# Optimization experiments

Measured on AMD Instinct MI355X. Metric: run time of the kernel, lower is better.

The kernel has to match this reference:

```python
import jax, jax.numpy as jnp
import numpy as np

N, J, P = 512, 20000, 8   # samples, genes (rna_count), covariates
DIM = J - 1               # pivot=True drops one column from the softmax logits


def setup_inputs() -> dict:
    key = jax.random.key(0)
    k0, k1, k2, k3, k4 = jax.random.split(key, 5)
    X = jax.random.normal(k0, (N, P), dtype=jnp.float32)
    # counts: non-negative integers stored as float (matches torch float64 Y of counts)
    Y = jnp.round(jax.random.uniform(k1, (N, J), dtype=jnp.float32) * 1000.0)
    mu = jax.random.normal(k2, (DIM,), dtype=jnp.float32)
    beta = jax.random.normal(k3, (P * DIM,), dtype=jnp.float32) * 0.1
    phi = jax.random.normal(k4, (J,), dtype=jnp.float32)
    return {"mu": mu, "beta": beta, "phi": phi, "X": X, "Y": Y}


def _nb_loglik(y, mean, disp):
    # NB with mean `mean` and dispersion `disp` (var = mean + disp*mean^2):
    # r = 1/disp, p = r/(r+mean)
    # log pmf = lgamma(y+r) - lgamma(r) - lgamma(y+1) + r*log(p) + y*log(1-p)
    r = 1.0 / disp
    log_rpm = jnp.log(r + mean)
    return (jax.lax.lgamma(y + r) - jax.lax.lgamma(r) - jax.lax.lgamma(y + 1.0)
            + r * (jnp.log(r) - log_rpm)
            + y * (jnp.log(mean) - log_rpm))


def reference(mu, beta, phi, X, Y):
    n, p = X.shape
    dim = mu.shape[0]
    beta_ = beta.reshape(p, dim)
    logits = mu + X @ beta_                                   # [N, J-1]
    logits = jnp.concatenate(
        [logits, jnp.zeros((n, 1), dtype=logits.dtype)], axis=1)  # pivot column of zeros -> [N, J]
    pi = jax.nn.softmax(logits, axis=1)                       # exp(logits - logsumexp)
    s = jnp.sum(Y, axis=1, keepdims=True)                     # [N, 1] total counts per sample
    mean = s * pi                                             # [N, J]
    disp = jax.nn.softplus(phi)                               # [J]
    log_lik = jnp.sum(_nb_loglik(Y, mean, disp))
    return log_lik.reshape(1)
```

## Files before the change

### kernel.cpp

```cpp
#include <hip/hip_runtime.h>

constexpr int N_SAMPLES = 512;
constexpr int J_GENES   = 20000;
constexpr int P_COV     = 8;
constexpr int DIM       = J_GENES - 1;
constexpr int BLOCK     = 256;
constexpr int NW        = BLOCK / 64;
constexpr int CHUNK     = 2048;
constexpr int NBJ       = 10;
constexpr int JPAD      = NBJ * CHUNK;
constexpr int NPART     = NBJ * N_SAMPLES;
constexpr int TABLE_N   = 1024;

constexpr size_t WS_RW    = 0;
constexpr size_t WS_MUP   = WS_RW    + JPAD;
constexpr size_t WS_BETAP = WS_MUP   + JPAD;
constexpr size_t WS_CVEC  = WS_BETAP + (size_t)P_COV * JPAD;
constexpr size_t WS_LGYT  = WS_CVEC  + JPAD;
constexpr size_t WS_SACC  = WS_LGYT  + TABLE_N;
constexpr size_t WS_EACC  = WS_SACC  + N_SAMPLES;
constexpr size_t WS_PART  = WS_EACC  + N_SAMPLES;
constexpr size_t WS_TOTAL = WS_PART  + NPART;

__device__ inline float wave_reduce_sum(float v) {
#pragma unroll
    for (int off = 32; off > 0; off >>= 1)
        v += __shfl_down(v, off, 64);
    return v;
}

__device__ inline float block_reduce_sum(float v, float* red) {
    const int t = threadIdx.x;
    float w = wave_reduce_sum(v);
    if ((t & 63) == 0) red[t >> 6] = w;
    __syncthreads();
    float b = 0.0f;
#pragma unroll
    for (int i = 0; i < NW; ++i) b += red[i];
    return b;
}

__device__ inline float lgamma_pos(float z) {
    float corr = 0.0f;
    if (z < 8.0f) {
        float p = z;
        p *= (z + 1.0f); p *= (z + 2.0f); p *= (z + 3.0f);
        p *= (z + 4.0f); p *= (z + 5.0f); p *= (z + 6.0f); p *= (z + 7.0f);
        corr = -__logf(p);
        z += 8.0f;
    }
    float lz  = __logf(z);
    float rz  = __builtin_amdgcn_rcpf(z);
    float rz2 = rz * rz;
    float ser = rz * fmaf(rz2, fmaf(rz2, 7.9365079365e-4f, -2.7777777778e-3f),
                          8.3333333333e-2f);
    return fmaf(z - 0.5f, lz, 0.91893853320467274f - z + ser + corr);
}

__device__ inline float4 logits4(const float* __restrict__ ws,
                                 const float* __restrict__ x, int j) {
    float4 lg = *(const float4*)(ws + WS_MUP + j);
#pragma unroll
    for (int p = 0; p < P_COV; ++p) {
        float4 bb = *(const float4*)(ws + WS_BETAP + (size_t)p * JPAD + j);
        lg.x = fmaf(x[p], bb.x, lg.x);
        lg.y = fmaf(x[p], bb.y, lg.y);
        lg.z = fmaf(x[p], bb.z, lg.z);
        lg.w = fmaf(x[p], bb.w, lg.w);
    }
    return lg;
}

__global__ __launch_bounds__(BLOCK) void prep_kernel(
    const float* __restrict__ mu, const float* __restrict__ beta,
    const float* __restrict__ phi, float* __restrict__ ws) {
    const int gid = blockIdx.x * BLOCK + threadIdx.x;
    if (gid < TABLE_N) ws[WS_LGYT + gid] = lgammaf((float)gid + 1.0f);
    if (gid < N_SAMPLES) { ws[WS_SACC + gid] = 0.0f; ws[WS_EACC + gid] = 0.0f; }
    if (gid >= JPAD) return;
    if (gid < J_GENES) {
        const int j = gid;
        float ph = phi[j];
        float sp = (ph > 20.0f) ? ph : log1pf(__expf(ph));
        float r  = 1.0f / sp;
        ws[WS_RW   + j] = r;
        ws[WS_CVEC + j] = fmaf(r, -__logf(sp), -lgammaf(r));
        ws[WS_MUP  + j] = (j < DIM) ? mu[j] : 0.0f;
#pragma unroll
        for (int p = 0; p < P_COV; ++p)
            ws[WS_BETAP + (size_t)p * JPAD + j] =
                (j < DIM) ? beta[p * DIM + j] : 0.0f;
    } else {
        ws[WS_RW   + gid] = 1.0f;
        ws[WS_CVEC + gid] = 0.0f;
        ws[WS_MUP  + gid] = 0.0f;
#pragma unroll
        for (int p = 0; p < P_COV; ++p)
            ws[WS_BETAP + (size_t)p * JPAD + gid] = 0.0f;
    }
}

__global__ __launch_bounds__(BLOCK) void rowsum_kernel(
    const float* __restrict__ X, const float* __restrict__ Y,
    float* __restrict__ ws) {
    const int n = blockIdx.y;
    const int t = threadIdx.x;
    const int j0 = blockIdx.x * CHUNK + t * 4;

    float x[P_COV];
#pragma unroll
    for (int p = 0; p < P_COV; ++p) x[p] = X[n * P_COV + p];
    const float* yrow = Y + (size_t)n * J_GENES;

    float s_acc = 0.0f, e_acc = 0.0f;
    for (int g = 0; g < 2; ++g) {
        const int j = j0 + g * (BLOCK * 4);
        if (j < J_GENES) {
            float4 y4 = *(const float4*)(yrow + j);
            float4 lg = logits4(ws, x, j);
            s_acc += (y4.x + y4.y) + (y4.z + y4.w);
            e_acc += (__expf(lg.x) + __expf(lg.y)) + (__expf(lg.z) + __expf(lg.w));
        }
    }

    __shared__ float red[NW];
    float s = block_reduce_sum(s_acc, red);
    __syncthreads();
    float e = block_reduce_sum(e_acc, red);
    if (t == 0) {
        atomicAdd(&ws[WS_SACC + n], s);
        atomicAdd(&ws[WS_EACC + n], e);
    }
}

__global__ __launch_bounds__(BLOCK) void loglik_kernel(
    const float* __restrict__ X, const float* __restrict__ Y,
    float* __restrict__ ws) {
    const int n = blockIdx.y;
    const int t = threadIdx.x;
    const int j0 = blockIdx.x * CHUNK + t * 4;

    __shared__ __align__(16) float tbl[TABLE_N];
    *(float4*)&tbl[t * 4] = *(const float4*)(ws + WS_LGYT + t * 4);

    float x[P_COV];
#pragma unroll
    for (int p = 0; p < P_COV; ++p) x[p] = X[n * P_COV + p];
    const float* yrow = Y + (size_t)n * J_GENES;

    const float s  = ws[WS_SACC + n];
    const float E  = ws[WS_EACC + n];
    const float sE = s / E;
    __syncthreads();

    float acc = 0.0f;
    for (int g = 0; g < 2; ++g) {
        const int j = j0 + g * (BLOCK * 4);
        if (j < J_GENES) {
            float4 y4 = *(const float4*)(yrow + j);
            float4 r4 = *(const float4*)(ws + WS_RW + j);
            float4 lg = logits4(ws, x, j);
#pragma unroll
            for (int e = 0; e < 4; ++e) {
                float y     = (&y4.x)[e];
                float r     = (&r4.x)[e];
                float logit = (&lg.x)[e];
                float mean  = sE * __expf(logit);
                float lrm   = __logf(r + mean);
                int   yi    = (int)(y + 0.5f);
                float lgy1  = (yi < TABLE_N) ? tbl[yi] : lgamma_pos(y + 1.0f);
                acc += lgamma_pos(y + r) - lgy1
                     + fmaf(-(y + r), lrm, y * logit);
            }
        }
    }

    __shared__ float red[NW];
    float b = block_reduce_sum(acc, red);
    if (t == 0) ws[WS_PART + (size_t)n * NBJ + blockIdx.x] = b;
}

__global__ __launch_bounds__(BLOCK) void final_kernel(
    const float* __restrict__ ws, float* __restrict__ out) {
    const int t = threadIdx.x;
    float acc = 0.0f;
    for (int i = t; i < NPART; i += BLOCK) acc += ws[WS_PART + i];
    for (int n = t; n < N_SAMPLES; n += BLOCK) {
        float s = ws[WS_SACC + n];
        float E = ws[WS_EACC + n];
        acc += s * (__logf(s) - __logf(E));
    }
    float cacc = 0.0f;
    for (int i = t; i < J_GENES; i += BLOCK) cacc += ws[WS_CVEC + i];
    acc += (float)N_SAMPLES * cacc;

    __shared__ float red[NW];
    float b = block_reduce_sum(acc, red);
    if (t == 0) out[0] = b;
}

__global__ __launch_bounds__(256) void nb_mono(
    const float* __restrict__ mu, const float* __restrict__ beta,
    const float* __restrict__ phi, const float* __restrict__ X,
    const float* __restrict__ Y, float* __restrict__ out) {
    const int n = blockIdx.x;
    const int t = threadIdx.x;
    __shared__ float red[4];
    __shared__ float sh_s, sh_lse, sh_logs;
    float x[P_COV];
#pragma unroll
    for (int p = 0; p < P_COV; ++p) x[p] = X[n * P_COV + p];
    const float* yrow = Y + (size_t)n * J_GENES;
    float s_acc = 0.0f, e_acc = 0.0f;
    for (int j = t; j < J_GENES; j += 256) {
        float logit = 0.0f;
        if (j < DIM) {
            logit = mu[j];
#pragma unroll
            for (int p = 0; p < P_COV; ++p)
                logit = fmaf(x[p], beta[p * DIM + j], logit);
        }
        s_acc += yrow[j];
        e_acc += __expf(logit);
    }
    float v = wave_reduce_sum(s_acc);
    if ((t & 63) == 0) red[t >> 6] = v;
    __syncthreads();
    if (t == 0) { float st = red[0]+red[1]+red[2]+red[3]; sh_s = st; sh_logs = __logf(st); }
    __syncthreads();
    v = wave_reduce_sum(e_acc);
    if ((t & 63) == 0) red[t >> 6] = v;
    __syncthreads();
    if (t == 0) sh_lse = __logf(red[0]+red[1]+red[2]+red[3]);
    __syncthreads();
    const float s = sh_s, logs = sh_logs, lse = sh_lse;
    float acc = 0.0f;
    for (int j = t; j < J_GENES; j += 256) {
        float logit = 0.0f;
        if (j < DIM) {
            logit = mu[j];
#pragma unroll
            for (int p = 0; p < P_COV; ++p)
                logit = fmaf(x[p], beta[p * DIM + j], logit);
        }
        float ph = phi[j];
        float sp = (ph > 20.0f) ? ph : log1pf(__expf(ph));
        float r  = 1.0f / sp;
        float y  = yrow[j];
        float lp = logit - lse;
        float mean = s * __expf(lp);
        float lrm  = __logf(r + mean);
        acc += lgamma_pos(y + r) - lgamma_pos(r) - lgamma_pos(y + 1.0f)
             + fmaf(r, -__logf(sp) - lrm, y * ((logs + lp) - lrm));
    }
    v = wave_reduce_sum(acc);
    if ((t & 63) == 0) red[t >> 6] = v;
    __syncthreads();
    if (t == 0) atomicAdd(out, (red[0]+red[1])+(red[2]+red[3]));
}

__global__ void zero_out_kernel(float* __restrict__ out) { out[0] = 0.0f; }

extern "C" void kernel_launch(void* const* d_in, const int* in_sizes, int n_in,
                              void* d_out, int out_size, void* d_ws, size_t ws_size,
                              hipStream_t stream) {
    const float* mu   = (const float*)d_in[0];
    const float* beta = (const float*)d_in[1];
    const float* phi  = (const float*)d_in[2];
    const float* X    = (const float*)d_in[3];
    const float* Y    = (const float*)d_in[4];
    float* out = (float*)d_out;
    float* ws  = (float*)d_ws;

    if (ws_size >= WS_TOTAL * sizeof(float)) {
        dim3 grid(NBJ, N_SAMPLES);
        prep_kernel<<<JPAD / BLOCK, BLOCK, 0, stream>>>(mu, beta, phi, ws);
        rowsum_kernel<<<grid, BLOCK, 0, stream>>>(X, Y, ws);
        loglik_kernel<<<grid, BLOCK, 0, stream>>>(X, Y, ws);
        final_kernel<<<1, BLOCK, 0, stream>>>(ws, out);
    } else {
        zero_out_kernel<<<1, 1, 0, stream>>>(out);
        nb_mono<<<N_SAMPLES, 256, 0, stream>>>(mu, beta, phi, X, Y, out);
    }
}
```

Baseline: 153.0 us.

## Compute logits once in row-tiled kernel and cache them as fp16

The rowsum kernel becomes logitE_kernel. It handles 16 rows per block and keeps mu and beta in registers, so those parameters are reused across rows instead of reloaded for each sample. It also writes the logits to the workspace as fp16, and loglik_kernel reads them back instead of recomputing the 8-term dot product and rereading beta. The cost is an extra 20 MB fp16 write plus a read, and lower logit precision, which feeds the exp and y*logit terms and may hurt accuracy.

```diff
diff --git a/kernel.cpp b/kernel.cpp
--- a/kernel.cpp
+++ b/kernel.cpp
@@ -1,4 +1,5 @@
 #include <hip/hip_runtime.h>
+#include <hip/hip_fp16.h>
 
 constexpr int N_SAMPLES = 512;
 constexpr int J_GENES   = 20000;
@@ -6,11 +7,18 @@
 constexpr int DIM       = J_GENES - 1;
 constexpr int BLOCK     = 256;
 constexpr int NW        = BLOCK / 64;
-constexpr int CHUNK     = 2048;
-constexpr int NBJ       = 10;
-constexpr int JPAD      = NBJ * CHUNK;
-constexpr int NPART     = NBJ * N_SAMPLES;
-constexpr int TABLE_N   = 1024;
+
+constexpr int GCHUNK = 1024;
+constexpr int NGC    = 20;
+constexpr int JPAD   = NGC * GCHUNK;
+constexpr int ROWT   = 16;
+constexpr int NRT    = N_SAMPLES / ROWT;
+
+constexpr int LCHUNK = 2048;
+constexpr int NBJ    = 10;
+constexpr int NPART  = NBJ * N_SAMPLES;
+
+constexpr int TABLE_N = 1024;
 
 constexpr size_t WS_RW    = 0;
 constexpr size_t WS_MUP   = WS_RW    + JPAD;
@@ -20,7 +28,8 @@
 constexpr size_t WS_SACC  = WS_LGYT  + TABLE_N;
 constexpr size_t WS_EACC  = WS_SACC  + N_SAMPLES;
 constexpr size_t WS_PART  = WS_EACC  + N_SAMPLES;
-constexpr size_t WS_TOTAL = WS_PART  + NPART;
+constexpr size_t WS_LOGH  = WS_PART  + NPART;
+constexpr size_t WS_TOTAL = WS_LOGH  + (size_t)N_SAMPLES * JPAD / 2;
 
 __device__ inline float wave_reduce_sum(float v) {
 #pragma unroll
@@ -55,20 +64,6 @@
     float ser = rz * fmaf(rz2, fmaf(rz2, 7.9365079365e-4f, -2.7777777778e-3f),
                           8.3333333333e-2f);
     return fmaf(z - 0.5f, lz, 0.91893853320467274f - z + ser + corr);
-}
-
-__device__ inline float4 logits4(const float* __restrict__ ws,
-                                 const float* __restrict__ x, int j) {
-    float4 lg = *(const float4*)(ws + WS_MUP + j);
-#pragma unroll
-    for (int p = 0; p < P_COV; ++p) {
-        float4 bb = *(const float4*)(ws + WS_BETAP + (size_t)p * JPAD + j);
-        lg.x = fmaf(x[p], bb.x, lg.x);
-        lg.y = fmaf(x[p], bb.y, lg.y);
-        lg.z = fmaf(x[p], bb.z, lg.z);
-        lg.w = fmaf(x[p], bb.w, lg.w);
-    }
-    return lg;
 }
 
 __global__ __launch_bounds__(BLOCK) void prep_kernel(
@@ -100,53 +95,90 @@
     }
 }
 
-__global__ __launch_bounds__(BLOCK) void rowsum_kernel(
+__global__ __launch_bounds__(BLOCK) void logitE_kernel(
     const float* __restrict__ X, const float* __restrict__ Y,
     float* __restrict__ ws) {
+    const int t    = threadIdx.x;
+    const int j    = blockIdx.x * GCHUNK + t * 4;
+    const int row0 = blockIdx.y * ROWT;
+    const bool valid = (j < J_GENES);
+
+    __shared__ __align__(16) float xs[ROWT * P_COV];
+    __shared__ float lds_s[ROWT][NW], lds_e[ROWT][NW];
+    if (t < ROWT * P_COV) xs[t] = X[row0 * P_COV + t];
+    __syncthreads();
+
+    const float4 zero4 = make_float4(0.f, 0.f, 0.f, 0.f);
+    float4 mu4 = valid ? *(const float4*)(ws + WS_MUP + j) : zero4;
+    float4 b0 = valid ? *(const float4*)(ws + WS_BETAP + 0 * JPAD + j) : zero4;
+    float4 b1 = valid ? *(const float4*)(ws + WS_BETAP + 1 * JPAD + j) : zero4;
+    float4 b2 = valid ? *(const float4*)(ws + WS_BETAP + 2 * JPAD + j) : zero4;
+    float4 b3 = valid ? *(const float4*)(ws + WS_BETAP + 3 * JPAD + j) : zero4;
+    float4 b4 = valid ? *(const float4*)(ws + WS_BETAP + 4 * JPAD + j) : zero4;
+    float4 b5 = valid ? *(const float4*)(ws + WS_BETAP + 5 * JPAD + j) : zero4;
+    float4 b6 = valid ? *(const float4*)(ws + WS_BETAP + 6 * JPAD + j) : zero4;
+    float4 b7 = valid ? *(const float4*)(ws + WS_BETAP + 7 * JPAD + j) : zero4;
+
+    __half* logh = (__half*)(ws + WS_LOGH);
+
+#pragma unroll 2
+    for (int r = 0; r < ROWT; ++r) {
+        const int n = row0 + r;
+        float4 xa = *(const float4*)&xs[r * P_COV + 0];
+        float4 xb = *(const float4*)&xs[r * P_COV + 4];
+
+        float4 lg = mu4;
+        lg.x = fmaf(xa.x, b0.x, lg.x); lg.y = fmaf(xa.x, b0.y, lg.y);
+        lg.z = fmaf(xa.x, b0.z, lg.z); lg.w = fmaf(xa.x, b0.w, lg.w);
+        lg.x = fmaf(xa.y, b1.x, lg.x); lg.y = fmaf(xa.y, b1.y, lg.y);
+        lg.z = fmaf(xa.y, b1.z, lg.z); lg.w = fmaf(xa.y, b1.w, lg.w);
+        lg.x = fmaf(xa.z, b2.x, lg.x); lg.y = fmaf(xa.z, b2.y, lg.y);
+        lg.z = fmaf(xa.z, b2.z, lg.z); lg.w = fmaf(xa.z, b2.w, lg.w);
+        lg.x = fmaf(xa.w, b3.x, lg.x); lg.y = fmaf(xa.w, b3.y, lg.y);
+        lg.z = fmaf(xa.w, b3.z, lg.z); lg.w = fmaf(xa.w, b3.w, lg.w);
+        lg.x = fmaf(xb.x, b4.x, lg.x); lg.y = fmaf(xb.x, b4.y, lg.y);
+        lg.z = fmaf(xb.x, b4.z, lg.z); lg.w = fmaf(xb.x, b4.w, lg.w);
+        lg.x = fmaf(xb.y, b5.x, lg.x); lg.y = fmaf(xb.y, b5.y, lg.y);
+        lg.z = fmaf(xb.y, b5.z, lg.z); lg.w = fmaf(xb.y, b5.w, lg.w);
+        lg.x = fmaf(xb.z, b6.x, lg.x); lg.y = fmaf(xb.z, b6.y, lg.y);
+        lg.z = fmaf(xb.z, b6.z, lg.z); lg.w = fmaf(xb.z, b6.w, lg.w);
+        lg.x = fmaf(xb.w, b7.x, lg.x); lg.y = fmaf(xb.w, b7.y, lg.y);
+        lg.z = fmaf(xb.w, b7.z, lg.z); lg.w = fmaf(xb.w, b7.w, lg.w);
+
+        float e_c = 0.0f, s_c = 0.0f;
+        if (valid) {
+            e_c = (__expf(lg.x) + __expf(lg.y)) + (__expf(lg.z) + __expf(lg.w));
+            float4 y4 = *(const float4*)(Y + (size_t)n * J_GENES + j);
+            s_c = (y4.x + y4.y) + (y4.z + y4.w);
+            __half2* dst = (__half2*)(logh + (size_t)n * JPAD + j);
+            dst[0] = __floats2half2_rn(lg.x, lg.y);
+            dst[1] = __floats2half2_rn(lg.z, lg.w);
+        }
+        float es = wave_reduce_sum(e_c);
+        float ss = wave_reduce_sum(s_c);
+        if ((t & 63) == 0) { lds_e[r][t >> 6] = es; lds_s[r][t >> 6] = ss; }
+    }
+    __syncthreads();
+    if (t < ROWT) {
+        float es = 0.f, ss = 0.f;
+#pragma unroll
+        for (int w = 0; w < NW; ++w) { es += lds_e[t][w]; ss += lds_s[t][w]; }
+        atomicAdd(&ws[WS_EACC + row0 + t], es);
+        atomicAdd(&ws[WS_SACC + row0 + t], ss);
+    }
+}
+
+__global__ __launch_bounds__(BLOCK) void loglik_kernel(
+    const float* __restrict__ Y, float* __restrict__ ws) {
     const int n = blockIdx.y;
     const int t = threadIdx.x;
-    const int j0 = blockIdx.x * CHUNK + t * 4;
-
-    float x[P_COV];
-#pragma unroll
-    for (int p = 0; p < P_COV; ++p) x[p] = X[n * P_COV + p];
-    const float* yrow = Y + (size_t)n * J_GENES;
-
-    float s_acc = 0.0f, e_acc = 0.0f;
-    for (int g = 0; g < 2; ++g) {
-        const int j = j0 + g * (BLOCK * 4);
-        if (j < J_GENES) {
-            float4 y4 = *(const float4*)(yrow + j);
-            float4 lg = logits4(ws, x, j);
-            s_acc += (y4.x + y4.y) + (y4.z + y4.w);
-            e_acc += (__expf(lg.x) + __expf(lg.y)) + (__expf(lg.z) + __expf(lg.w));
-        }
-    }
-
-    __shared__ float red[NW];
-    float s = block_reduce_sum(s_acc, red);
-    __syncthreads();
-    float e = block_reduce_sum(e_acc, red);
-    if (t == 0) {
-        atomicAdd(&ws[WS_SACC + n], s);
-        atomicAdd(&ws[WS_EACC + n], e);
-    }
-}
-
-__global__ __launch_bounds__(BLOCK) void loglik_kernel(
-    const float* __restrict__ X, const float* __restrict__ Y,
-    float* __restrict__ ws) {
-    const int n = blockIdx.y;
-    const int t = threadIdx.x;
-    const int j0 = blockIdx.x * CHUNK + t * 4;
+    const int j0 = blockIdx.x * LCHUNK + t * 4;
 
     __shared__ __align__(16) float tbl[TABLE_N];
     *(float4*)&tbl[t * 4] = *(const float4*)(ws + WS_LGYT + t * 4);
 
-    float x[P_COV];
-#pragma unroll
-    for (int p = 0; p < P_COV; ++p) x[p] = X[n * P_COV + p];
     const float* yrow = Y + (size_t)n * J_GENES;
+    const __half* lrow = (const __half*)(ws + WS_LOGH) + (size_t)n * JPAD;
 
     const float s  = ws[WS_SACC + n];
     const float E  = ws[WS_EACC + n];
@@ -159,12 +191,15 @@
         if (j < J_GENES) {
             float4 y4 = *(const float4*)(yrow + j);
             float4 r4 = *(const float4*)(ws + WS_RW + j);
-            float4 lg = logits4(ws, x, j);
+            const __half2* lp = (const __half2*)(lrow + j);
+            float2 l01 = __half22float2(lp[0]);
+            float2 l23 = __half22float2(lp[1]);
+            float lgv[4] = {l01.x, l01.y, l23.x, l23.y};
 #pragma unroll
             for (int e = 0; e < 4; ++e) {
                 float y     = (&y4.x)[e];
                 float r     = (&r4.x)[e];
-                float logit = (&lg.x)[e];
+                float logit = lgv[e];
                 float mean  = sE * __expf(logit);
                 float lrm   = __logf(r + mean);
                 int   yi    = (int)(y + 0.5f);
@@ -273,10 +308,9 @@
     float* ws  = (float*)d_ws;
 
     if (ws_size >= WS_TOTAL * sizeof(float)) {
-        dim3 grid(NBJ, N_SAMPLES);
         prep_kernel<<<JPAD / BLOCK, BLOCK, 0, stream>>>(mu, beta, phi, ws);
-        rowsum_kernel<<<grid, BLOCK, 0, stream>>>(X, Y, ws);
-        loglik_kernel<<<grid, BLOCK, 0, stream>>>(X, Y, ws);
+        logitE_kernel<<<dim3(NGC, NRT), BLOCK, 0, stream>>>(X, Y, ws);
+        loglik_kernel<<<dim3(NBJ, N_SAMPLES), BLOCK, 0, stream>>>(Y, ws);
         final_kernel<<<1, BLOCK, 0, stream>>>(ws, out);
     } else {
         zero_out_kernel<<<1, 1, 0, stream>>>(out);
```

After: 150.8 us. Within noise of the previous version (-1.5%).
